# Optimization experiments

Hardware: AMD Instinct MI355X
Metric: run time of the kernel (lower is better)

## Reference

```python
import jax, jax.numpy as jnp
import numpy as np

N_NODES = 100000
N_EDGES = 1600000
IN_DIM = 165
HIDDEN = 128
OUT_DIM = 2


def gcn_conv(x, W, b, src, dst, n_nodes):
    """PyG GCNConv: h = x @ W; add self-loops; sym-normalized scatter-add; + bias."""
    h = x @ W  # [N, F_out]
    loop = jnp.arange(n_nodes, dtype=src.dtype)
    src_f = jnp.concatenate([src, loop])  # [E + N]
    dst_f = jnp.concatenate([dst, loop])
    deg = jax.ops.segment_sum(jnp.ones(src_f.shape[0], dtype=h.dtype), dst_f,
                              num_segments=n_nodes)  # in-degree incl. self-loop
    dinv = jnp.where(deg > 0, jax.lax.rsqrt(deg), jnp.zeros_like(deg))
    norm = dinv[src_f] * dinv[dst_f]  # [E + N]
    msg = h[src_f] * norm[:, None]  # gather + scale, [E+N, F_out]
    out = jax.ops.segment_sum(msg, dst_f, num_segments=n_nodes)  # scatter-add
    return out + b


def setup_inputs() -> dict:
    key = jax.random.key(0)
    k_x, k_e, k_w1, k_b1, k_w2, k_b2 = jax.random.split(key, 6)
    x = jax.random.normal(k_x, (N_NODES, IN_DIM), dtype=jnp.float32)
    edge_index = jax.random.randint(k_e, (2, N_EDGES), 0, N_NODES, dtype=jnp.int64)
    # Glorot-like init for linear weights, zeros for bias (PyG defaults)
    W1 = jax.random.normal(k_w1, (IN_DIM, HIDDEN), dtype=jnp.float32) / np.sqrt(IN_DIM)
    b1 = jnp.zeros((HIDDEN,), dtype=jnp.float32)
    W2 = jax.random.normal(k_w2, (HIDDEN, OUT_DIM), dtype=jnp.float32) / np.sqrt(HIDDEN)
    b2 = jnp.zeros((OUT_DIM,), dtype=jnp.float32)
    return {"x": x, "edge_index": edge_index, "W1": W1, "b1": b1, "W2": W2, "b2": b2}


def reference(x, edge_index, W1, b1, W2, b2):
    src, dst = edge_index[0], edge_index[1]
    h = gcn_conv(x, W1, b1, src, dst, N_NODES)
    h = jax.nn.relu(h)
    # dropout: eval mode (training=False) -> identity
    out = gcn_conv(h, W2, b2, src, dst, N_NODES)
    return out
```

## Files before the change

kernel.cpp:

```cpp
#include <hip/hip_runtime.h>
#include <hip/hip_fp16.h>

#define N_NODES 100000
#define N_EDGES 1600000
#define IN_DIM  165
#define HIDDEN  128
#define OUT_DIM 2

#define NBKT 196
#define CHUNK 4096
#define NCHUNK ((N_EDGES + CHUNK - 1) / CHUNK)
#define PADCAP 10240
#define KPAD 176

typedef _Float16 half8_t __attribute__((ext_vector_type(8)));
typedef _Float16 half4_t __attribute__((ext_vector_type(4)));
typedef float floatx4 __attribute__((ext_vector_type(4)));
typedef float floatx4_a4 __attribute__((ext_vector_type(4), aligned(4)));


__global__ __launch_bounds__(512) void k_part2(const int* __restrict__ src,
                                               const int* __restrict__ dst,
                                               int* __restrict__ bcnt,
                                               unsigned* __restrict__ arena) {
    __shared__ int hist[256];
    __shared__ int gbase[256];

    int t = threadIdx.x;
    int e0 = blockIdx.x * CHUNK;
    int nE = N_EDGES - e0; if (nE > CHUNK) nE = CHUNK;
    int n4 = nE >> 2;
    const int4* dst4 = (const int4*)(dst + e0);
    const int4* src4 = (const int4*)(src + e0);

    if (t < 256) hist[t] = 0;
    __syncthreads();

    for (int i = t; i < n4; i += 512) {
        int4 d = dst4[i];
        atomicAdd(&hist[d.x >> 9], 1);
        atomicAdd(&hist[d.y >> 9], 1);
        atomicAdd(&hist[d.z >> 9], 1);
        atomicAdd(&hist[d.w >> 9], 1);
    }
    __syncthreads();

    if (t < NBKT) gbase[t] = t * PADCAP + atomicAdd(&bcnt[t], hist[t]);
    if (t < 256) hist[t] = 0;
    __syncthreads();

    for (int i = t; i < n4; i += 512) {
        int4 d = dst4[i];
        int4 s = src4[i];
        #pragma unroll
        for (int j = 0; j < 4; j++) {
            int dd = (j == 0) ? d.x : (j == 1) ? d.y : (j == 2) ? d.z : d.w;
            int ss = (j == 0) ? s.x : (j == 1) ? s.y : (j == 2) ? s.z : s.w;
            int bk = dd >> 9;
            unsigned entry = (unsigned)ss | ((unsigned)(dd & 511) << 17);
            int idx = atomicAdd(&hist[bk], 1);
            arena[gbase[bk] + idx] = entry;
        }
    }
}


__global__ __launch_bounds__(256) void k_btot(const int* __restrict__ bcnt,
                                              int* __restrict__ bucketptr) {
    __shared__ int wsum[4];
    int t = threadIdx.x, lane = t & 63, wid = t >> 6;
    int v = (t < NBKT) ? bcnt[t] : 0;
    int inc = v;
    #pragma unroll
    for (int off = 1; off < 64; off <<= 1) {
        int y = __shfl_up(inc, off);
        if (lane >= off) inc += y;
    }
    if (lane == 63) wsum[wid] = inc;
    __syncthreads();
    if (t == 0) {
        int acc = 0;
        #pragma unroll
        for (int w = 0; w < 4; w++) { int tv = wsum[w]; wsum[w] = acc; acc += tv; }
    }
    __syncthreads();
    int excl = wsum[wid] + inc - v;
    if (t <= NBKT) bucketptr[t] = (t < NBKT) ? excl : N_EDGES;
}


__global__ __launch_bounds__(1024) void k_sort3(const unsigned* __restrict__ arena,
                                                const int* __restrict__ bcnt,
                                                const int* __restrict__ bucketptr,
                                                int* __restrict__ csr,
                                                int* __restrict__ rowptr,
                                                float* __restrict__ dinv) {
    __shared__ int cnt[512];
    __shared__ int cur[512];
    __shared__ int wsum[4];
    int b = blockIdx.x;
    int n0 = b << 9;
    int t = threadIdx.x;
    int lane = t & 63, wid = t >> 6;
    int total = bcnt[b];
    int abase = b * PADCAP;
    int dbase = bucketptr[b];
    int nt4 = total >> 2;
    const uint4* arena4 = (const uint4*)(arena + abase);

    if (t < 512) cnt[t] = 0;
    __syncthreads();
    for (int p = t; p < nt4; p += 1024) {
        uint4 e = arena4[p];
        atomicAdd(&cnt[e.x >> 17], 1);
        atomicAdd(&cnt[e.y >> 17], 1);
        atomicAdd(&cnt[e.z >> 17], 1);
        atomicAdd(&cnt[e.w >> 17], 1);
    }
    {
        int p = (nt4 << 2) + t;
        if (p < total) atomicAdd(&cnt[arena[abase + p] >> 17], 1);
    }
    __syncthreads();

    int c0 = 0, c1 = 0, s = 0, inc = 0;
    if (t < 256) {
        c0 = cnt[2 * t];
        c1 = cnt[2 * t + 1];
        s = c0 + c1;
        inc = s;
        #pragma unroll
        for (int off = 1; off < 64; off <<= 1) {
            int y = __shfl_up(inc, off);
            if (lane >= off) inc += y;
        }
        if (lane == 63) wsum[wid] = inc;
    }
    __syncthreads();
    if (t == 0) {
        int acc = 0;
        #pragma unroll
        for (int w = 0; w < 4; w++) { int tv = wsum[w]; wsum[w] = acc; acc += tv; }
    }
    __syncthreads();
    if (t < 256) {
        int base = dbase + wsum[wid] + (inc - s);
        cur[2 * t] = base;
        cur[2 * t + 1] = base + c0;
        int node0 = n0 + 2 * t;
        if (node0 < N_NODES) {
            rowptr[node0] = base;
            dinv[node0] = rsqrtf((float)(c0 + 1));
        }
        if (node0 + 1 < N_NODES) {
            rowptr[node0 + 1] = base + c0;
            dinv[node0 + 1] = rsqrtf((float)(c1 + 1));
        }
    }
    if (b == NBKT - 1 && t == 0) rowptr[N_NODES] = N_EDGES;
    __syncthreads();

    for (int p = t; p < nt4; p += 1024) {
        uint4 e = arena4[p];
        #pragma unroll
        for (int j = 0; j < 4; j++) {
            unsigned entry = (j == 0) ? e.x : (j == 1) ? e.y : (j == 2) ? e.z : e.w;
            int local = (int)(entry >> 17);
            int sv = (int)(entry & 0x1FFFFu);
            int pos = atomicAdd(&cur[local], 1);
            csr[pos] = sv;
        }
    }
    {
        int p = (nt4 << 2) + t;
        if (p < total) {
            unsigned entry = arena[abase + p];
            int local = (int)(entry >> 17);
            int sv = (int)(entry & 0x1FFFFu);
            int pos = atomicAdd(&cur[local], 1);
            csr[pos] = sv;
        }
    }
}


__global__ void k_w1t(const float* __restrict__ W1, _Float16* __restrict__ w1t) {
    int idx = blockIdx.x * 256 + threadIdx.x;
    if (idx < HIDDEN * KPAD) {
        int c = idx / KPAD, k = idx - c * KPAD;
        float v = (k < IN_DIM) ? W1[k * HIDDEN + c] : 0.f;
        w1t[idx] = (_Float16)v;
    }
}


__global__ __launch_bounds__(256) void k_gemm1(const float* __restrict__ x,
                                               const _Float16* __restrict__ w1t,
                                               const float* __restrict__ dinv,
                                               _Float16* __restrict__ h1s) {
    int t = threadIdx.x;
    int wid = t >> 6, lane = t & 63;
    int row0 = (blockIdx.x * 4 + wid) * 16;
    if (row0 >= N_NODES) return;
    int m = lane & 15;
    int quad = lane >> 4;
    const float* xrow = x + (size_t)(row0 + m) * IN_DIM;

    floatx4 acc[8];
    #pragma unroll
    for (int i = 0; i < 8; i++) acc[i] = (floatx4)(0.f);

    #pragma unroll
    for (int kc = 0; kc < 5; kc++) {
        int kb = kc * 32 + quad * 8;
        floatx4_a4 va = *(const floatx4_a4*)(xrow + kb);
        floatx4_a4 vb = *(const floatx4_a4*)(xrow + kb + 4);
        half8_t a;
        #pragma unroll
        for (int j = 0; j < 4; j++) a[j] = (_Float16)va[j];
        #pragma unroll
        for (int j = 0; j < 4; j++) a[4 + j] = (_Float16)vb[j];
        #pragma unroll
        for (int cb = 0; cb < 8; cb++) {
            int col = cb * 16 + m;
            half8_t bf = *(const half8_t*)&w1t[col * KPAD + kb];
            acc[cb] = __builtin_amdgcn_mfma_f32_16x16x32_f16(a, bf, acc[cb], 0, 0, 0);
        }
    }
    {
        int kb = 160 + quad * 4;
        half4_t a;
        #pragma unroll
        for (int j = 0; j < 4; j++)
            a[j] = (kb + j < IN_DIM) ? (_Float16)xrow[kb + j] : (_Float16)0.f;
        #pragma unroll
        for (int cb = 0; cb < 8; cb++) {
            int col = cb * 16 + m;
            half4_t bf = *(const half4_t*)&w1t[col * KPAD + kb];
            acc[cb] = __builtin_amdgcn_mfma_f32_16x16x16f16(a, bf, acc[cb], 0, 0, 0);
        }
    }
    float dv[4];
    #pragma unroll
    for (int r = 0; r < 4; r++) dv[r] = dinv[row0 + quad * 4 + r];
    #pragma unroll
    for (int cb = 0; cb < 8; cb++) {
        #pragma unroll
        for (int r = 0; r < 4; r++) {
            h1s[(size_t)(row0 + quad * 4 + r) * HIDDEN + cb * 16 + m] =
                (_Float16)(acc[cb][r] * dv[r]);
        }
    }
}


__global__ __launch_bounds__(256) void k_agg1(const _Float16* __restrict__ h1,
                                              const int* __restrict__ rowptr,
                                              const int* __restrict__ csr,
                                              const float* __restrict__ dinv,
                                              const float* __restrict__ b1,
                                              const float* __restrict__ W2,
                                              float2* __restrict__ h2s) {
    int wid = threadIdx.x >> 6, lane = threadIdx.x & 63;
    int el = lane & 15;
    int es = lane >> 4;
    int node = blockIdx.x * 4 + wid;

    float acc[8];
    {
        half8_t v = *(const half8_t*)(h1 + (size_t)node * HIDDEN + el * 8);
        #pragma unroll
        for (int j = 0; j < 8; j++) acc[j] = (es == 0) ? (float)v[j] : 0.f;
    }

    int p0 = rowptr[node], p1 = rowptr[node + 1];
    int p = p0 + es;
    for (; p + 4 < p1; p += 8) {
        int sA = csr[p];
        int sB = csr[p + 4];
        half8_t vA = *(const half8_t*)(h1 + (size_t)sA * HIDDEN + el * 8);
        half8_t vB = *(const half8_t*)(h1 + (size_t)sB * HIDDEN + el * 8);
        #pragma unroll
        for (int j = 0; j < 8; j++) acc[j] += (float)vA[j];
        #pragma unroll
        for (int j = 0; j < 8; j++) acc[j] += (float)vB[j];
    }
    if (p < p1) {
        int s = csr[p];
        half8_t v = *(const half8_t*)(h1 + (size_t)s * HIDDEN + el * 8);
        #pragma unroll
        for (int j = 0; j < 8; j++) acc[j] += (float)v[j];
    }

    #pragma unroll
    for (int j = 0; j < 8; j++) {
        acc[j] += __shfl_xor(acc[j], 16);
        acc[j] += __shfl_xor(acc[j], 32);
    }

    float di = dinv[node];
    float4 bb0 = ((const float4*)b1)[el * 2];
    float4 bb1 = ((const float4*)b1)[el * 2 + 1];
    float bv[8] = {bb0.x, bb0.y, bb0.z, bb0.w, bb1.x, bb1.y, bb1.z, bb1.w};
    float a0 = 0.f, a1 = 0.f;
    #pragma unroll
    for (int j = 0; j < 8; j++) {
        float z = fmaf(di, acc[j], bv[j]);
        float r = fmaxf(z, 0.f);
        float2 w = ((const float2*)W2)[el * 8 + j];
        a0 = fmaf(r, w.x, a0);
        a1 = fmaf(r, w.y, a1);
    }
    #pragma unroll
    for (int off = 8; off; off >>= 1) {
        a0 += __shfl_xor(a0, off);
        a1 += __shfl_xor(a1, off);
    }
    if (lane == 0) h2s[node] = make_float2(di * a0, di * a1);
}


__global__ __launch_bounds__(256) void k_agg2(const float2* __restrict__ h2s,
                                              const int* __restrict__ rowptr,
                                              const int* __restrict__ csr,
                                              const float* __restrict__ dinv,
                                              const float* __restrict__ b2,
                                              float2* __restrict__ out) {
    int wid = threadIdx.x >> 6, lane = threadIdx.x & 63;
    int sub = lane >> 4, el = lane & 15;
    int node = blockIdx.x * 16 + wid * 4 + sub;
    int p0 = rowptr[node], p1 = rowptr[node + 1];
    float ax = 0.f, ay = 0.f;
    for (int p = p0 + el; p < p1; p += 16) {
        float2 g = h2s[csr[p]];
        ax += g.x;
        ay += g.y;
    }
    #pragma unroll
    for (int off = 8; off; off >>= 1) {
        ax += __shfl_xor(ax, off);
        ay += __shfl_xor(ay, off);
    }
    if (el == 0) {
        float2 self = h2s[node];
        float di = dinv[node];
        out[node] = make_float2(fmaf(di, self.x + ax, b2[0]),
                                fmaf(di, self.y + ay, b2[1]));
    }
}


extern "C" void kernel_launch(void* const* d_in, const int* in_sizes, int n_in,
                              void* d_out, int out_size, void* d_ws, size_t ws_size,
                              hipStream_t stream) {
    const float* x  = (const float*)d_in[0];
    const int*   ei = (const int*)d_in[1];
    const float* W1 = (const float*)d_in[2];
    const float* b1 = (const float*)d_in[3];
    const float* W2 = (const float*)d_in[4];
    const float* b2 = (const float*)d_in[5];
    float* out = (float*)d_out;

    const int* src = ei;
    const int* dst = ei + N_EDGES;

    char* ws = (char*)d_ws;
    size_t off = 0;
    auto alloc = [&](size_t bytes) -> void* {
        void* p = ws + off;
        off += (bytes + 255) & ~(size_t)255;
        return p;
    };
    _Float16* h1s    = (_Float16*)alloc((size_t)N_NODES * HIDDEN * 2);
    float*    dinv   = (float*)   alloc((size_t)N_NODES * 4);
    int*      rowptr = (int*)     alloc((size_t)(N_NODES + 1) * 4);
    int*      bcnt   = (int*)     alloc((size_t)NBKT * 4);
    int*      bktptr = (int*)     alloc((size_t)(NBKT + 1) * 4);
    unsigned* arena  = (unsigned*)alloc((size_t)NBKT * PADCAP * 4);
    int*      csr    = (int*)     alloc((size_t)N_EDGES * 4);
    _Float16* w1t    = (_Float16*)alloc((size_t)HIDDEN * KPAD * 2);
    float2*   h2s    = (float2*)  alloc((size_t)N_NODES * 8);

    (void)hipMemsetAsync(bcnt, 0, (size_t)NBKT * 4, stream);
    k_w1t<<<(HIDDEN * KPAD + 255) / 256, 256, 0, stream>>>(W1, w1t);
    k_part2<<<NCHUNK, 512, 0, stream>>>(src, dst, bcnt, arena);
    k_btot<<<1, 256, 0, stream>>>(bcnt, bktptr);
    k_sort3<<<NBKT, 1024, 0, stream>>>(arena, bcnt, bktptr, csr, rowptr, dinv);
    k_gemm1<<<(N_NODES / 16 + 3) / 4, 256, 0, stream>>>(x, w1t, dinv, h1s);
    k_agg1<<<N_NODES / 4, 256, 0, stream>>>(h1s, rowptr, csr, dinv, b1, W2, h2s);
    k_agg2<<<N_NODES / 16, 256, 0, stream>>>(h2s, rowptr, csr, dinv, b2, (float2*)out);
}
```

Baseline: 250.1 us.

## Slice h1 features into 16-wide column panels for cache-friendly aggregation

The GEMM output h1 is stored as 8 separate feature slices of 16 halves per node instead of row-major 128-wide rows. The first aggregation kernel now runs one block per node group per slice, so each pass gathers from a 3.2 MB slice that can stay in cache rather than the full 25.6 MB array. Each slice produces a partial layer-2 projection, and a new small kernel sums the slices and applies dinv. The cost is reading the CSR indices 8 times, an extra kernel launch, and partial results written into the reused arena buffer.

```diff
diff --git a/kernel.cpp b/kernel.cpp
--- a/kernel.cpp
+++ b/kernel.cpp
@@ -12,6 +12,7 @@
 #define NCHUNK ((N_EDGES + CHUNK - 1) / CHUNK)
 #define PADCAP 10240
 #define KPAD 176
+#define NSLICE 8
 
 typedef _Float16 half8_t __attribute__((ext_vector_type(8)));
 typedef _Float16 half4_t __attribute__((ext_vector_type(4)));
@@ -247,7 +248,7 @@
     for (int cb = 0; cb < 8; cb++) {
         #pragma unroll
         for (int r = 0; r < 4; r++) {
-            h1s[(size_t)(row0 + quad * 4 + r) * HIDDEN + cb * 16 + m] =
+            h1s[((size_t)cb * N_NODES + (row0 + quad * 4 + r)) * 16 + m] =
                 (_Float16)(acc[cb][r] * dv[r]);
         }
     }
@@ -260,63 +261,75 @@
                                               const float* __restrict__ dinv,
                                               const float* __restrict__ b1,
                                               const float* __restrict__ W2,
-                                              float2* __restrict__ h2s) {
-    int wid = threadIdx.x >> 6, lane = threadIdx.x & 63;
-    int el = lane & 15;
-    int es = lane >> 4;
-    int node = blockIdx.x * 4 + wid;
+                                              float2* __restrict__ h2part) {
+    int t = threadIdx.x;
+    int wid = t >> 6, lane = t & 63;
+    int s  = blockIdx.x & 7;
+    int g  = blockIdx.x >> 3;
+    int half = lane >> 5;
+    int l  = lane & 31;
+    int fl = l & 1;
+    int es = l >> 1;
+    int node = g * 8 + wid * 2 + half;
+
+    const _Float16* hs = h1 + (size_t)s * N_NODES * 16;
 
     float acc[8];
     {
-        half8_t v = *(const half8_t*)(h1 + (size_t)node * HIDDEN + el * 8);
+        half8_t v = *(const half8_t*)(hs + (size_t)node * 16 + fl * 8);
         #pragma unroll
         for (int j = 0; j < 8; j++) acc[j] = (es == 0) ? (float)v[j] : 0.f;
     }
 
     int p0 = rowptr[node], p1 = rowptr[node + 1];
-    int p = p0 + es;
-    for (; p + 4 < p1; p += 8) {
-        int sA = csr[p];
-        int sB = csr[p + 4];
-        half8_t vA = *(const half8_t*)(h1 + (size_t)sA * HIDDEN + el * 8);
-        half8_t vB = *(const half8_t*)(h1 + (size_t)sB * HIDDEN + el * 8);
-        #pragma unroll
-        for (int j = 0; j < 8; j++) acc[j] += (float)vA[j];
-        #pragma unroll
-        for (int j = 0; j < 8; j++) acc[j] += (float)vB[j];
-    }
-    if (p < p1) {
-        int s = csr[p];
-        half8_t v = *(const half8_t*)(h1 + (size_t)s * HIDDEN + el * 8);
+    for (int p = p0 + es; p < p1; p += 16) {
+        int sv = __builtin_nontemporal_load(&csr[p]);
+        half8_t v = *(const half8_t*)(hs + (size_t)sv * 16 + fl * 8);
         #pragma unroll
         for (int j = 0; j < 8; j++) acc[j] += (float)v[j];
     }
 
     #pragma unroll
     for (int j = 0; j < 8; j++) {
+        acc[j] += __shfl_xor(acc[j], 2);
+        acc[j] += __shfl_xor(acc[j], 4);
+        acc[j] += __shfl_xor(acc[j], 8);
         acc[j] += __shfl_xor(acc[j], 16);
-        acc[j] += __shfl_xor(acc[j], 32);
     }
 
     float di = dinv[node];
-    float4 bb0 = ((const float4*)b1)[el * 2];
-    float4 bb1 = ((const float4*)b1)[el * 2 + 1];
+    float4 bb0 = ((const float4*)b1)[(s * 16 + fl * 8) >> 2];
+    float4 bb1 = ((const float4*)b1)[((s * 16 + fl * 8) >> 2) + 1];
     float bv[8] = {bb0.x, bb0.y, bb0.z, bb0.w, bb1.x, bb1.y, bb1.z, bb1.w};
     float a0 = 0.f, a1 = 0.f;
     #pragma unroll
     for (int j = 0; j < 8; j++) {
         float z = fmaf(di, acc[j], bv[j]);
         float r = fmaxf(z, 0.f);
-        float2 w = ((const float2*)W2)[el * 8 + j];
+        float2 w = ((const float2*)W2)[s * 16 + fl * 8 + j];
         a0 = fmaf(r, w.x, a0);
         a1 = fmaf(r, w.y, a1);
     }
-    #pragma unroll
-    for (int off = 8; off; off >>= 1) {
-        a0 += __shfl_xor(a0, off);
-        a1 += __shfl_xor(a1, off);
-    }
-    if (lane == 0) h2s[node] = make_float2(di * a0, di * a1);
+    a0 += __shfl_xor(a0, 1);
+    a1 += __shfl_xor(a1, 1);
+    if (l == 0) h2part[(size_t)s * N_NODES + node] = make_float2(a0, a1);
+}
+
+
+__global__ __launch_bounds__(256) void k_h2sum(const float2* __restrict__ h2part,
+                                               const float* __restrict__ dinv,
+                                               float2* __restrict__ h2s) {
+    int n = blockIdx.x * 256 + threadIdx.x;
+    if (n >= N_NODES) return;
+    float ax = 0.f, ay = 0.f;
+    #pragma unroll
+    for (int s = 0; s < NSLICE; s++) {
+        float2 v = h2part[(size_t)s * N_NODES + n];
+        ax += v.x;
+        ay += v.y;
+    }
+    float di = dinv[n];
+    h2s[n] = make_float2(di * ax, di * ay);
 }
 
 
@@ -380,6 +393,7 @@
     int*      csr    = (int*)     alloc((size_t)N_EDGES * 4);
     _Float16* w1t    = (_Float16*)alloc((size_t)HIDDEN * KPAD * 2);
     float2*   h2s    = (float2*)  alloc((size_t)N_NODES * 8);
+    float2*   h2part = (float2*)arena;
 
     (void)hipMemsetAsync(bcnt, 0, (size_t)NBKT * 4, stream);
     k_w1t<<<(HIDDEN * KPAD + 255) / 256, 256, 0, stream>>>(W1, w1t);
@@ -387,6 +401,7 @@
     k_btot<<<1, 256, 0, stream>>>(bcnt, bktptr);
     k_sort3<<<NBKT, 1024, 0, stream>>>(arena, bcnt, bktptr, csr, rowptr, dinv);
     k_gemm1<<<(N_NODES / 16 + 3) / 4, 256, 0, stream>>>(x, w1t, dinv, h1s);
-    k_agg1<<<N_NODES / 4, 256, 0, stream>>>(h1s, rowptr, csr, dinv, b1, W2, h2s);
+    k_agg1<<<(N_NODES / 8) * NSLICE, 256, 0, stream>>>(h1s, rowptr, csr, dinv, b1, W2, h2part);
+    k_h2sum<<<(N_NODES + 255) / 256, 256, 0, stream>>>(h2part, dinv, h2s);
     k_agg2<<<N_NODES / 16, 256, 0, stream>>>(h2s, rowptr, csr, dinv, b2, (float2*)out);
 }
```

Measured after the change: 366.1 us. 1.46x slower.

## Drop bucket prefix-sum kernel via padded CSR with start/end arrays; unroll agg1

Applied to the files above, without the earlier changes.

Removes the single-block bucket prefix-sum kernel by giving each destination bucket a fixed PADCAP-sized region in the CSR array, with separate rowstart/rowend arrays replacing rowptr. This saves one kernel launch and its serialization point. The agg1 gather loop is also unrolled from 2 to 4 independent neighbor loads per lane, using nontemporal loads for csr indices. In exchange the CSR array grows with padding gaps, and more index arrays are read per node.

```diff
diff --git a/kernel.cpp b/kernel.cpp
--- a/kernel.cpp
+++ b/kernel.cpp
@@ -65,35 +65,11 @@
 }
 
 
-__global__ __launch_bounds__(256) void k_btot(const int* __restrict__ bcnt,
-                                              int* __restrict__ bucketptr) {
-    __shared__ int wsum[4];
-    int t = threadIdx.x, lane = t & 63, wid = t >> 6;
-    int v = (t < NBKT) ? bcnt[t] : 0;
-    int inc = v;
-    #pragma unroll
-    for (int off = 1; off < 64; off <<= 1) {
-        int y = __shfl_up(inc, off);
-        if (lane >= off) inc += y;
-    }
-    if (lane == 63) wsum[wid] = inc;
-    __syncthreads();
-    if (t == 0) {
-        int acc = 0;
-        #pragma unroll
-        for (int w = 0; w < 4; w++) { int tv = wsum[w]; wsum[w] = acc; acc += tv; }
-    }
-    __syncthreads();
-    int excl = wsum[wid] + inc - v;
-    if (t <= NBKT) bucketptr[t] = (t < NBKT) ? excl : N_EDGES;
-}
-
-
-__global__ __launch_bounds__(1024) void k_sort3(const unsigned* __restrict__ arena,
+__global__ __launch_bounds__(1024) void k_sort4(const unsigned* __restrict__ arena,
                                                 const int* __restrict__ bcnt,
-                                                const int* __restrict__ bucketptr,
                                                 int* __restrict__ csr,
-                                                int* __restrict__ rowptr,
+                                                int* __restrict__ rowstart,
+                                                int* __restrict__ rowend,
                                                 float* __restrict__ dinv) {
     __shared__ int cnt[512];
     __shared__ int cur[512];
@@ -104,7 +80,7 @@
     int lane = t & 63, wid = t >> 6;
     int total = bcnt[b];
     int abase = b * PADCAP;
-    int dbase = bucketptr[b];
+    int dbase = b * PADCAP;
     int nt4 = total >> 2;
     const uint4* arena4 = (const uint4*)(arena + abase);
 
@@ -149,15 +125,16 @@
         cur[2 * t + 1] = base + c0;
         int node0 = n0 + 2 * t;
         if (node0 < N_NODES) {
-            rowptr[node0] = base;
+            rowstart[node0] = base;
+            rowend[node0] = base + c0;
             dinv[node0] = rsqrtf((float)(c0 + 1));
         }
         if (node0 + 1 < N_NODES) {
-            rowptr[node0 + 1] = base + c0;
+            rowstart[node0 + 1] = base + c0;
+            rowend[node0 + 1] = base + c0 + c1;
             dinv[node0 + 1] = rsqrtf((float)(c1 + 1));
         }
     }
-    if (b == NBKT - 1 && t == 0) rowptr[N_NODES] = N_EDGES;
     __syncthreads();
 
     for (int p = t; p < nt4; p += 1024) {
@@ -255,7 +232,8 @@
 
 
 __global__ __launch_bounds__(256) void k_agg1(const _Float16* __restrict__ h1,
-                                              const int* __restrict__ rowptr,
+                                              const int* __restrict__ rowstart,
+                                              const int* __restrict__ rowend,
                                               const int* __restrict__ csr,
                                               const float* __restrict__ dinv,
                                               const float* __restrict__ b1,
@@ -273,20 +251,28 @@
         for (int j = 0; j < 8; j++) acc[j] = (es == 0) ? (float)v[j] : 0.f;
     }
 
-    int p0 = rowptr[node], p1 = rowptr[node + 1];
+    int p0 = rowstart[node], p1 = rowend[node];
     int p = p0 + es;
-    for (; p + 4 < p1; p += 8) {
-        int sA = csr[p];
-        int sB = csr[p + 4];
-        half8_t vA = *(const half8_t*)(h1 + (size_t)sA * HIDDEN + el * 8);
-        half8_t vB = *(const half8_t*)(h1 + (size_t)sB * HIDDEN + el * 8);
-        #pragma unroll
-        for (int j = 0; j < 8; j++) acc[j] += (float)vA[j];
-        #pragma unroll
-        for (int j = 0; j < 8; j++) acc[j] += (float)vB[j];
-    }
-    if (p < p1) {
-        int s = csr[p];
+    for (; p + 12 < p1; p += 16) {
+        int s0 = __builtin_nontemporal_load(&csr[p]);
+        int s1 = __builtin_nontemporal_load(&csr[p + 4]);
+        int s2 = __builtin_nontemporal_load(&csr[p + 8]);
+        int s3 = __builtin_nontemporal_load(&csr[p + 12]);
+        half8_t v0 = *(const half8_t*)(h1 + (size_t)s0 * HIDDEN + el * 8);
+        half8_t v1 = *(const half8_t*)(h1 + (size_t)s1 * HIDDEN + el * 8);
+        half8_t v2 = *(const half8_t*)(h1 + (size_t)s2 * HIDDEN + el * 8);
+        half8_t v3 = *(const half8_t*)(h1 + (size_t)s3 * HIDDEN + el * 8);
+        #pragma unroll
+        for (int j = 0; j < 8; j++) acc[j] += (float)v0[j];
+        #pragma unroll
+        for (int j = 0; j < 8; j++) acc[j] += (float)v1[j];
+        #pragma unroll
+        for (int j = 0; j < 8; j++) acc[j] += (float)v2[j];
+        #pragma unroll
+        for (int j = 0; j < 8; j++) acc[j] += (float)v3[j];
+    }
+    for (; p < p1; p += 4) {
+        int s = __builtin_nontemporal_load(&csr[p]);
         half8_t v = *(const half8_t*)(h1 + (size_t)s * HIDDEN + el * 8);
         #pragma unroll
         for (int j = 0; j < 8; j++) acc[j] += (float)v[j];
@@ -321,7 +307,8 @@
 
 
 __global__ __launch_bounds__(256) void k_agg2(const float2* __restrict__ h2s,
-                                              const int* __restrict__ rowptr,
+                                              const int* __restrict__ rowstart,
+                                              const int* __restrict__ rowend,
                                               const int* __restrict__ csr,
                                               const float* __restrict__ dinv,
                                               const float* __restrict__ b2,
@@ -329,7 +316,7 @@
     int wid = threadIdx.x >> 6, lane = threadIdx.x & 63;
     int sub = lane >> 4, el = lane & 15;
     int node = blockIdx.x * 16 + wid * 4 + sub;
-    int p0 = rowptr[node], p1 = rowptr[node + 1];
+    int p0 = rowstart[node], p1 = rowend[node];
     float ax = 0.f, ay = 0.f;
     for (int p = p0 + el; p < p1; p += 16) {
         float2 g = h2s[csr[p]];
@@ -371,22 +358,21 @@
         off += (bytes + 255) & ~(size_t)255;
         return p;
     };
-    _Float16* h1s    = (_Float16*)alloc((size_t)N_NODES * HIDDEN * 2);
-    float*    dinv   = (float*)   alloc((size_t)N_NODES * 4);
-    int*      rowptr = (int*)     alloc((size_t)(N_NODES + 1) * 4);
-    int*      bcnt   = (int*)     alloc((size_t)NBKT * 4);
-    int*      bktptr = (int*)     alloc((size_t)(NBKT + 1) * 4);
-    unsigned* arena  = (unsigned*)alloc((size_t)NBKT * PADCAP * 4);
-    int*      csr    = (int*)     alloc((size_t)N_EDGES * 4);
-    _Float16* w1t    = (_Float16*)alloc((size_t)HIDDEN * KPAD * 2);
-    float2*   h2s    = (float2*)  alloc((size_t)N_NODES * 8);
+    _Float16* h1s      = (_Float16*)alloc((size_t)N_NODES * HIDDEN * 2);
+    float*    dinv     = (float*)   alloc((size_t)N_NODES * 4);
+    int*      rowstart = (int*)     alloc((size_t)N_NODES * 4);
+    int*      rowend   = (int*)     alloc((size_t)N_NODES * 4);
+    int*      bcnt     = (int*)     alloc((size_t)NBKT * 4);
+    unsigned* arena    = (unsigned*)alloc((size_t)NBKT * PADCAP * 4);
+    int*      csr      = (int*)     alloc((size_t)NBKT * PADCAP * 4);
+    _Float16* w1t      = (_Float16*)alloc((size_t)HIDDEN * KPAD * 2);
+    float2*   h2s      = (float2*)  alloc((size_t)N_NODES * 8);
 
     (void)hipMemsetAsync(bcnt, 0, (size_t)NBKT * 4, stream);
     k_w1t<<<(HIDDEN * KPAD + 255) / 256, 256, 0, stream>>>(W1, w1t);
     k_part2<<<NCHUNK, 512, 0, stream>>>(src, dst, bcnt, arena);
-    k_btot<<<1, 256, 0, stream>>>(bcnt, bktptr);
-    k_sort3<<<NBKT, 1024, 0, stream>>>(arena, bcnt, bktptr, csr, rowptr, dinv);
+    k_sort4<<<NBKT, 1024, 0, stream>>>(arena, bcnt, csr, rowstart, rowend, dinv);
     k_gemm1<<<(N_NODES / 16 + 3) / 4, 256, 0, stream>>>(x, w1t, dinv, h1s);
-    k_agg1<<<N_NODES / 4, 256, 0, stream>>>(h1s, rowptr, csr, dinv, b1, W2, h2s);
-    k_agg2<<<N_NODES / 16, 256, 0, stream>>>(h2s, rowptr, csr, dinv, b2, (float2*)out);
-}
+    k_agg1<<<N_NODES / 4, 256, 0, stream>>>(h1s, rowstart, rowend, csr, dinv, b1, W2, h2s);
+    k_agg2<<<N_NODES / 16, 256, 0, stream>>>(h2s, rowstart, rowend, csr, dinv, b2, (float2*)out);
+}
```

Measured after the change: 257.0 us. 2.8% more time.
